# Performance work log

Measured on AMD Instinct MI355X. Metric: run time of the kernel, lower is better.

The kernel has to match this reference:

```python
import jax, jax.numpy as jnp
import numpy as np

B, S, H, D = 8, 1024, 16, 64  # batch, seq, heads, d_heads; hidden = H*D = 1024

def setup_inputs() -> dict:
    key = jax.random.key(0)
    ks = jax.random.split(key, 7)
    sc = 1.0 / np.sqrt(D)
    return {
        "sequences": jax.random.normal(ks[0], (B, S, H * D), dtype=jnp.float32),
        "Wq": jax.random.normal(ks[1], (H, D, D), dtype=jnp.float32) * sc,
        "bq": jax.random.normal(ks[2], (H, D), dtype=jnp.float32) * 0.01,
        "Wk": jax.random.normal(ks[3], (H, D, D), dtype=jnp.float32) * sc,
        "bk": jax.random.normal(ks[4], (H, D), dtype=jnp.float32) * 0.01,
        "Wv": jax.random.normal(ks[5], (H, D, D), dtype=jnp.float32) * sc,
        "bv": jax.random.normal(ks[6], (H, D), dtype=jnp.float32) * 0.01,
    }

def reference(sequences, Wq, bq, Wk, bk, Wv, bv):
    # sequences: [B, S, H*D] -> [B, S, H, D] (head h uses slice h*D:(h+1)*D)
    x = sequences.reshape(B, S, H, D)
    # per-head Linear: y = x @ W.T + b  (torch convention)
    q = jnp.einsum("bshd,hed->bshe", x, Wq) + bq
    k = jnp.einsum("bshd,hed->bshe", x, Wk) + bk
    v = jnp.einsum("bshd,hed->bshe", x, Wv) + bv
    scores = jnp.einsum("bqhd,bkhd->bhqk", q, k) / jnp.sqrt(jnp.float32(D))
    attn = jax.nn.softmax(scores, axis=-1)
    out = jnp.einsum("bhqk,bkhd->bqhd", attn, v)  # [B, S, H, D]
    return out.reshape(B, S, H * D)  # hstack over heads == reshape
```

## Files before the change

### kernel.cpp

```cpp
#include <hip/hip_runtime.h>
#include <hip/hip_bf16.h>


typedef __attribute__((ext_vector_type(8))) short short8;
typedef __attribute__((ext_vector_type(4))) float f32x4;
typedef __attribute__((ext_vector_type(16))) float f32x16;
typedef __attribute__((ext_vector_type(2))) unsigned int u32x2;
typedef __attribute__((ext_vector_type(4))) unsigned int u32x4;

#define MFMA32 __builtin_amdgcn_mfma_f32_32x32x16_bf16

#define QSCALE 0.1803368801111204f

__device__ __forceinline__ unsigned cvt_pk(float lo, float hi) {
  unsigned r;
  asm("v_cvt_pk_bf16_f32 %0, %1, %2" : "=v"(r) : "v"(lo), "v"(hi));
  return r;
}
__device__ __forceinline__ void pl32_swap(unsigned &a, unsigned &b) {
  asm("v_permlane32_swap_b32 %0, %1" : "+v"(a), "+v"(b));
}
__device__ __forceinline__ void pack_cd(const f32x16& p, short8& lo, short8& hi8) {
  unsigned d0 = cvt_pk(p[0],  p[1]);
  unsigned d2 = cvt_pk(p[4],  p[5]);
  pl32_swap(d0, d2);
  unsigned d1 = cvt_pk(p[2],  p[3]);
  unsigned d3 = cvt_pk(p[6],  p[7]);
  pl32_swap(d1, d3);
  u32x4 a = {d0, d1, d2, d3};
  unsigned e0 = cvt_pk(p[8],  p[9]);
  unsigned e2 = cvt_pk(p[12], p[13]);
  pl32_swap(e0, e2);
  unsigned e1 = cvt_pk(p[10], p[11]);
  unsigned e3 = cvt_pk(p[14], p[15]);
  pl32_swap(e1, e3);
  u32x4 b = {e0, e1, e2, e3};
  lo  = __builtin_bit_cast(short8, a);
  hi8 = __builtin_bit_cast(short8, b);
}
__device__ __forceinline__ void lds_barrier() {
  asm volatile("s_waitcnt lgkmcnt(0)" ::: "memory");
  __builtin_amdgcn_s_barrier();
}

__global__ __launch_bounds__(512) void kv_proj_kernel(
    const float* __restrict__ x,
    const float* __restrict__ Wk, const float* __restrict__ bk,
    const float* __restrict__ Wv, const float* __restrict__ bv,
    unsigned short* __restrict__ kv_ws)
{
  __shared__ unsigned short x_lds[128][72];
  __shared__ unsigned short wk_lds[64][72];
  __shared__ unsigned short wv_lds[64][72];

  const int h   = blockIdx.x & 15;
  const int tb  = blockIdx.x >> 4;
  const int tid = threadIdx.x;
  const int w   = tid >> 6;
  const int l   = tid & 63;
  const int hi  = l >> 5;
  const int cc  = l & 31;

  {
    const int r = tid >> 2, s = tid & 3;
    const float* xs = x + (size_t)(tb * 128 + r) * 1024 + h * 64 + s * 16;
    f32x4 v0 = *(const f32x4*)xs;
    f32x4 v1 = *(const f32x4*)(xs + 4);
    f32x4 v2 = *(const f32x4*)(xs + 8);
    f32x4 v3 = *(const f32x4*)(xs + 12);
    u32x4 d0 = {cvt_pk(v0[0], v0[1]), cvt_pk(v0[2], v0[3]),
                cvt_pk(v1[0], v1[1]), cvt_pk(v1[2], v1[3])};
    u32x4 d1 = {cvt_pk(v2[0], v2[1]), cvt_pk(v2[2], v2[3]),
                cvt_pk(v3[0], v3[1]), cvt_pk(v3[2], v3[3])};
    *(u32x4*)&x_lds[r][s * 16]     = d0;
    *(u32x4*)&x_lds[r][s * 16 + 8] = d1;
  }
  {
    const int r = tid >> 3, s = tid & 7;
    const float* wsk = Wk + (size_t)h * 4096 + r * 64 + s * 8;
    const float* wsv = Wv + (size_t)h * 4096 + r * 64 + s * 8;
    f32x4 k0 = *(const f32x4*)wsk;
    f32x4 k1 = *(const f32x4*)(wsk + 4);
    u32x4 dk = {cvt_pk(k0[0], k0[1]), cvt_pk(k0[2], k0[3]),
                cvt_pk(k1[0], k1[1]), cvt_pk(k1[2], k1[3])};
    *(u32x4*)&wk_lds[r][s * 8] = dk;
    f32x4 m0 = *(const f32x4*)wsv;
    f32x4 m1 = *(const f32x4*)(wsv + 4);
    u32x4 dv = {cvt_pk(m0[0], m0[1]), cvt_pk(m0[2], m0[3]),
                cvt_pk(m1[0], m1[1]), cvt_pk(m1[2], m1[3])};
    *(u32x4*)&wv_lds[r][s * 8] = dv;
  }
  __syncthreads();

  const int b = tb >> 3;
  unsigned short* kvt = kv_ws + (size_t)(b * 16 + h) * 131072
                              + (size_t)(tb & 7) * 16384;

  if (w < 4) {
    const int eb = w >> 1, cb = w & 1;
    const float* bkb = bk + h * 64 + eb * 32 + 4 * hi;
    f32x4 bk0 = *(const f32x4*)(bkb);
    f32x4 bk1 = *(const f32x4*)(bkb + 8);
    f32x4 bk2 = *(const f32x4*)(bkb + 16);
    f32x4 bk3 = *(const f32x4*)(bkb + 24);
#pragma unroll
    for (int sub = 0; sub < 2; ++sub) {
      f32x16 kkT = {};
#pragma unroll
      for (int ks = 0; ks < 4; ++ks) {
        short8 aW = *(const short8*)&wk_lds[eb * 32 + cc][ks * 16 + hi * 8];
        short8 bX = *(const short8*)&x_lds[sub * 64 + cb * 32 + cc][ks * 16 + hi * 8];
        kkT = MFMA32(aW, bX, kkT, 0, 0, 0);
      }
#pragma unroll
      for (int r = 0; r < 16; ++r) {
        const float bb = (r >> 2) == 0 ? bk0[r & 3] :
                         (r >> 2) == 1 ? bk1[r & 3] :
                         (r >> 2) == 2 ? bk2[r & 3] : bk3[r & 3];
        kkT[r] += bb;
      }
      short8 klo, khi;
      pack_cd(kkT, klo, khi);
      const int slot = 256 * eb + 64 * cb + l;
      *(short8*)&kvt[sub * 8192 + slot * 8]         = klo;
      *(short8*)&kvt[sub * 8192 + (slot + 128) * 8] = khi;
    }
  } else {
    const int tb32 = (w - 4) >> 1, db = (w - 4) & 1;
    const float bvv = bv[h * 64 + db * 32 + cc];
#pragma unroll
    for (int sub = 0; sub < 2; ++sub) {
      f32x16 vvC = {};
#pragma unroll
      for (int ks = 0; ks < 4; ++ks) {
        short8 aX = *(const short8*)&x_lds[sub * 64 + tb32 * 32 + cc][ks * 16 + hi * 8];
        short8 bW = *(const short8*)&wv_lds[db * 32 + cc][ks * 16 + hi * 8];
        vvC = MFMA32(aX, bW, vvC, 0, 0, 0);
      }
#pragma unroll
      for (int r = 0; r < 16; ++r) vvC[r] += bvv;
      short8 vlo, vhi;
      pack_cd(vvC, vlo, vhi);
      const int slot = 256 * tb32 + 64 * db + l;
      *(short8*)&kvt[sub * 8192 + 4096 + slot * 8]         = vlo;
      *(short8*)&kvt[sub * 8192 + 4096 + (slot + 128) * 8] = vhi;
    }
  }
}

__global__ __launch_bounds__(512, 4) void attn_kernel(
    const float* __restrict__ x,
    const float* __restrict__ Wq, const float* __restrict__ bq,
    const unsigned short* __restrict__ kv_ws,
    float* __restrict__ out)
{
  __shared__ __align__(16) char lds[32768];

  const int logical = (blockIdx.x & 7) * 64 + (blockIdx.x >> 3);
  const int qt = logical & 3;
  const int bh = logical >> 2;
  const int b  = bh >> 4;
  const int h  = bh & 15;
  const unsigned short* kvb = kv_ws + (size_t)bh * 131072;

  const int tid = threadIdx.x;
  const int w   = tid >> 6;
  const int l   = tid & 63;
  const int hi  = l >> 5;
  const int cc  = l & 31;

  const unsigned short* sgp = kvb + tid * 8;
  char* wbp = lds + tid * 16;

  short8 st[2];
#pragma unroll
  for (int j = 0; j < 2; ++j) st[j] = *(const short8*)(sgp + j * 4096);

  unsigned short* wq_l = (unsigned short*)lds;
  unsigned short* xh_l = (unsigned short*)(lds + 9216);

  {
    const int r = tid >> 3, s = tid & 7;
    const float* ws = Wq + h * 4096 + r * 64 + s * 8;
    f32x4 v0 = *(const f32x4*)ws;
    f32x4 v1 = *(const f32x4*)(ws + 4);
    u32x4 d = {cvt_pk(v0[0], v0[1]), cvt_pk(v0[2], v0[3]),
               cvt_pk(v1[0], v1[1]), cvt_pk(v1[2], v1[3])};
    *(u32x4*)&wq_l[r * 72 + s * 8] = d;
  }

  short8 qf[4];
  f32x16 qa0 = {}, qa1 = {};
#pragma unroll
  for (int p = 0; p < 2; ++p) {
    {
      const int r = tid >> 2, s = tid & 3;
      const float* xs = x + ((size_t)(b * 1024 + qt * 256 + p * 128 + r)) * 1024
                          + h * 64 + s * 16;
      f32x4 v0 = *(const f32x4*)xs;
      f32x4 v1 = *(const f32x4*)(xs + 4);
      f32x4 v2 = *(const f32x4*)(xs + 8);
      f32x4 v3 = *(const f32x4*)(xs + 12);
      u32x4 d0 = {cvt_pk(v0[0], v0[1]), cvt_pk(v0[2], v0[3]),
                  cvt_pk(v1[0], v1[1]), cvt_pk(v1[2], v1[3])};
      u32x4 d1 = {cvt_pk(v2[0], v2[1]), cvt_pk(v2[2], v2[3]),
                  cvt_pk(v3[0], v3[1]), cvt_pk(v3[2], v3[3])};
      *(u32x4*)&xh_l[r * 72 + s * 16]     = d0;
      *(u32x4*)&xh_l[r * 72 + s * 16 + 8] = d1;
    }
    lds_barrier();
    if ((w >> 2) == p) {
      const int tl = (w & 3) * 32 + cc;
#pragma unroll
      for (int c = 0; c < 4; ++c) {
        short8 xf  = *(const short8*)&xh_l[tl * 72 + c * 16 + hi * 8];
        short8 alo = *(const short8*)&wq_l[cc * 72 + c * 16 + hi * 8];
        short8 ahi = *(const short8*)&wq_l[(32 + cc) * 72 + c * 16 + hi * 8];
        qa0 = MFMA32(alo, xf, qa0, 0, 0, 0);
        qa1 = MFMA32(ahi, xf, qa1, 0, 0, 0);
      }
    }
    lds_barrier();
  }
  {
#pragma unroll
    for (int r = 0; r < 16; ++r) {
      const int e = (r & 3) + 8 * (r >> 2) + 4 * hi;
      qa0[r] = (qa0[r] + bq[h * 64 + e]) * QSCALE;
      qa1[r] = (qa1[r] + bq[h * 64 + 32 + e]) * QSCALE;
    }
    pack_cd(qa0, qf[0], qf[1]);
    pack_cd(qa1, qf[2], qf[3]);
  }

#pragma unroll
  for (int j = 0; j < 2; ++j) *(short8*)(wbp + j * 8192) = st[j];
#pragma unroll
  for (int j = 0; j < 2; ++j) st[j] = *(const short8*)(sgp + 8192 + j * 4096);
  lds_barrier();

  f32x16 ot0 = {}; f32x16 ot1 = {};
  float lsum = 0.f;

  for (int kv = 0; kv < 16; ++kv) {
    if (kv < 15) {
      char* d = wbp + ((kv + 1) & 1) * 16384;
#pragma unroll
      for (int j = 0; j < 2; ++j) *(short8*)(d + j * 8192) = st[j];
      if (kv < 14) {
        const unsigned short* s = sgp + (size_t)(kv + 2) * 8192;
#pragma unroll
        for (int j = 0; j < 2; ++j) st[j] = *(const short8*)(s + j * 4096);
      }
    }
    const char* kb_ = lds + (kv & 1) * 16384;
    const char* vb_ = kb_ + 8192;

    f32x16 s0 = {}; f32x16 s1 = {};
    __builtin_amdgcn_s_setprio(1);
#pragma unroll
    for (int c = 0; c < 4; ++c) {
      s0 = MFMA32(*(const short8*)(kb_ + (c * 128 + l) * 16),      qf[c], s0, 0, 0, 0);
      s1 = MFMA32(*(const short8*)(kb_ + (c * 128 + 64 + l) * 16), qf[c], s1, 0, 0, 0);
    }
    __builtin_amdgcn_s_setprio(0);

    float ps0 = 0.f, ps1 = 0.f;
#pragma unroll
    for (int i = 0; i < 16; ++i) { s0[i] = __builtin_amdgcn_exp2f(s0[i]); ps0 += s0[i]; }
#pragma unroll
    for (int i = 0; i < 16; ++i) { s1[i] = __builtin_amdgcn_exp2f(s1[i]); ps1 += s1[i]; }
    lsum += ps0 + ps1;

#pragma unroll
    for (int kb = 0; kb < 2; ++kb) {
      short8 pa0, pa1;
      pack_cd(kb ? s1 : s0, pa0, pa1);

      const int c20 = kb * 2, c21 = kb * 2 + 1;
      __builtin_amdgcn_s_setprio(1);
      ot0 = MFMA32(*(const short8*)(vb_ + (c20 * 128 + l) * 16),      pa0, ot0, 0, 0, 0);
      ot1 = MFMA32(*(const short8*)(vb_ + (c20 * 128 + 64 + l) * 16), pa0, ot1, 0, 0, 0);
      ot0 = MFMA32(*(const short8*)(vb_ + (c21 * 128 + l) * 16),      pa1, ot0, 0, 0, 0);
      ot1 = MFMA32(*(const short8*)(vb_ + (c21 * 128 + 64 + l) * 16), pa1, ot1, 0, 0, 0);
      __builtin_amdgcn_s_setprio(0);
    }
    lds_barrier();
  }

  const float lt  = lsum + __shfl_xor(lsum, 32, 64);
  const float inv = 1.0f / lt;
  const int s_row = qt * 256 + w * 32 + cc;
  float* op = out + ((size_t)(b * 1024 + s_row) << 10) + h * 64;
#pragma unroll
  for (int rg = 0; rg < 4; ++rg) {
    const int d0 = 8 * rg + 4 * hi;
    f32x4 v0, v1;
#pragma unroll
    for (int j = 0; j < 4; ++j) {
      v0[j] = ot0[rg * 4 + j] * inv;
      v1[j] = ot1[rg * 4 + j] * inv;
    }
    *(f32x4*)(op + d0)      = v0;
    *(f32x4*)(op + 32 + d0) = v1;
  }
}

extern "C" void kernel_launch(void* const* d_in, const int* in_sizes, int n_in,
                              void* d_out, int out_size, void* d_ws, size_t ws_size,
                              hipStream_t stream) {
  const float* x  = (const float*)d_in[0];
  const float* Wq = (const float*)d_in[1];
  const float* bq = (const float*)d_in[2];
  const float* Wk = (const float*)d_in[3];
  const float* bk = (const float*)d_in[4];
  const float* Wv = (const float*)d_in[5];
  const float* bv = (const float*)d_in[6];
  float* out = (float*)d_out;

  unsigned short* kv_ws = (unsigned short*)d_ws;

  kv_proj_kernel<<<1024, 512, 0, stream>>>(x, Wk, bk, Wv, bv, kv_ws);
  attn_kernel<<<512, 512, 0, stream>>>(x, Wq, bq, kv_ws, out);
}
```

Before: 67.21 us.

## Move Q projection into the projection kernel and load precomputed Q fragments

The Q projection moves out of the attention kernel into the first kernel, which now computes Q, K and V per 128-row tile, stores Q pre-scaled in bf16 fragment layout, and rebalances the work so all 8 waves do one tile of each. The attention kernel then loads Q fragments straight from workspace instead of reading x and Wq, converting them, and running an LDS-staged MFMA prologue with barriers. This shortens the attention kernel's prologue. In exchange it adds a bf16 Q round-trip through global memory (16 MB workspace) and more work and LDS in the projection kernel.

```diff
diff --git a/kernel.cpp b/kernel.cpp
--- a/kernel.cpp
+++ b/kernel.cpp
@@ -5,7 +5,6 @@
 typedef __attribute__((ext_vector_type(8))) short short8;
 typedef __attribute__((ext_vector_type(4))) float f32x4;
 typedef __attribute__((ext_vector_type(16))) float f32x16;
-typedef __attribute__((ext_vector_type(2))) unsigned int u32x2;
 typedef __attribute__((ext_vector_type(4))) unsigned int u32x4;
 
 #define MFMA32 __builtin_amdgcn_mfma_f32_32x32x16_bf16
@@ -43,13 +42,16 @@
   __builtin_amdgcn_s_barrier();
 }
 
-__global__ __launch_bounds__(512) void kv_proj_kernel(
+__global__ __launch_bounds__(512) void qkv_proj_kernel(
     const float* __restrict__ x,
+    const float* __restrict__ Wq, const float* __restrict__ bq,
     const float* __restrict__ Wk, const float* __restrict__ bk,
     const float* __restrict__ Wv, const float* __restrict__ bv,
+    unsigned short* __restrict__ q_ws,
     unsigned short* __restrict__ kv_ws)
 {
   __shared__ unsigned short x_lds[128][72];
+  __shared__ unsigned short wq_lds[64][72];
   __shared__ unsigned short wk_lds[64][72];
   __shared__ unsigned short wv_lds[64][72];
 
@@ -77,8 +79,14 @@
   }
   {
     const int r = tid >> 3, s = tid & 7;
+    const float* wsq = Wq + (size_t)h * 4096 + r * 64 + s * 8;
     const float* wsk = Wk + (size_t)h * 4096 + r * 64 + s * 8;
     const float* wsv = Wv + (size_t)h * 4096 + r * 64 + s * 8;
+    f32x4 q0 = *(const f32x4*)wsq;
+    f32x4 q1 = *(const f32x4*)(wsq + 4);
+    u32x4 dq = {cvt_pk(q0[0], q0[1]), cvt_pk(q0[2], q0[3]),
+                cvt_pk(q1[0], q1[1]), cvt_pk(q1[2], q1[3])};
+    *(u32x4*)&wq_lds[r][s * 8] = dq;
     f32x4 k0 = *(const f32x4*)wsk;
     f32x4 k1 = *(const f32x4*)(wsk + 4);
     u32x4 dk = {cvt_pk(k0[0], k0[1]), cvt_pk(k0[2], k0[3]),
@@ -93,64 +101,86 @@
   __syncthreads();
 
   const int b = tb >> 3;
-  unsigned short* kvt = kv_ws + (size_t)(b * 16 + h) * 131072
-                              + (size_t)(tb & 7) * 16384;
-
-  if (w < 4) {
-    const int eb = w >> 1, cb = w & 1;
-    const float* bkb = bk + h * 64 + eb * 32 + 4 * hi;
-    f32x4 bk0 = *(const f32x4*)(bkb);
-    f32x4 bk1 = *(const f32x4*)(bkb + 8);
-    f32x4 bk2 = *(const f32x4*)(bkb + 16);
-    f32x4 bk3 = *(const f32x4*)(bkb + 24);
-#pragma unroll
-    for (int sub = 0; sub < 2; ++sub) {
-      f32x16 kkT = {};
-#pragma unroll
-      for (int ks = 0; ks < 4; ++ks) {
-        short8 aW = *(const short8*)&wk_lds[eb * 32 + cc][ks * 16 + hi * 8];
-        short8 bX = *(const short8*)&x_lds[sub * 64 + cb * 32 + cc][ks * 16 + hi * 8];
-        kkT = MFMA32(aW, bX, kkT, 0, 0, 0);
-      }
-#pragma unroll
-      for (int r = 0; r < 16; ++r) {
-        const float bb = (r >> 2) == 0 ? bk0[r & 3] :
-                         (r >> 2) == 1 ? bk1[r & 3] :
-                         (r >> 2) == 2 ? bk2[r & 3] : bk3[r & 3];
-        kkT[r] += bb;
-      }
-      short8 klo, khi;
-      pack_cd(kkT, klo, khi);
-      const int slot = 256 * eb + 64 * cb + l;
-      *(short8*)&kvt[sub * 8192 + slot * 8]         = klo;
-      *(short8*)&kvt[sub * 8192 + (slot + 128) * 8] = khi;
-    }
-  } else {
-    const int tb32 = (w - 4) >> 1, db = (w - 4) & 1;
-    const float bvv = bv[h * 64 + db * 32 + cc];
-#pragma unroll
-    for (int sub = 0; sub < 2; ++sub) {
-      f32x16 vvC = {};
-#pragma unroll
-      for (int ks = 0; ks < 4; ++ks) {
-        short8 aX = *(const short8*)&x_lds[sub * 64 + tb32 * 32 + cc][ks * 16 + hi * 8];
-        short8 bW = *(const short8*)&wv_lds[db * 32 + cc][ks * 16 + hi * 8];
-        vvC = MFMA32(aX, bW, vvC, 0, 0, 0);
-      }
-#pragma unroll
-      for (int r = 0; r < 16; ++r) vvC[r] += bvv;
-      short8 vlo, vhi;
-      pack_cd(vvC, vlo, vhi);
-      const int slot = 256 * tb32 + 64 * db + l;
-      *(short8*)&kvt[sub * 8192 + 4096 + slot * 8]         = vlo;
-      *(short8*)&kvt[sub * 8192 + 4096 + (slot + 128) * 8] = vhi;
-    }
+  const int eb  = (w >> 2) & 1;
+  const int cb  = (w >> 1) & 1;
+  const int sub = w & 1;
+  const int tidx = (tb & 7) * 2 + sub;
+  unsigned short* kvt = kv_ws + (size_t)(b * 16 + h) * 131072 + (size_t)tidx * 8192;
+  unsigned short* qtt = q_ws  + (size_t)(b * 16 + h) * 65536  + (size_t)tidx * 4096;
+  const int slot = 256 * eb + 64 * cb + l;
+
+  {
+    f32x16 acc = {};
+#pragma unroll
+    for (int ks = 0; ks < 4; ++ks) {
+      short8 aW = *(const short8*)&wq_lds[eb * 32 + cc][ks * 16 + hi * 8];
+      short8 bX = *(const short8*)&x_lds[sub * 64 + cb * 32 + cc][ks * 16 + hi * 8];
+      acc = MFMA32(aW, bX, acc, 0, 0, 0);
+    }
+    const float* bb = bq + h * 64 + eb * 32 + 4 * hi;
+    f32x4 b0 = *(const f32x4*)(bb);
+    f32x4 b1 = *(const f32x4*)(bb + 8);
+    f32x4 b2 = *(const f32x4*)(bb + 16);
+    f32x4 b3 = *(const f32x4*)(bb + 24);
+#pragma unroll
+    for (int r = 0; r < 16; ++r) {
+      const float bz = (r >> 2) == 0 ? b0[r & 3] :
+                       (r >> 2) == 1 ? b1[r & 3] :
+                       (r >> 2) == 2 ? b2[r & 3] : b3[r & 3];
+      acc[r] = (acc[r] + bz) * QSCALE;
+    }
+    short8 lo, hi8;
+    pack_cd(acc, lo, hi8);
+    *(short8*)&qtt[slot * 8]         = lo;
+    *(short8*)&qtt[(slot + 128) * 8] = hi8;
+  }
+
+  {
+    f32x16 acc = {};
+#pragma unroll
+    for (int ks = 0; ks < 4; ++ks) {
+      short8 aW = *(const short8*)&wk_lds[eb * 32 + cc][ks * 16 + hi * 8];
+      short8 bX = *(const short8*)&x_lds[sub * 64 + cb * 32 + cc][ks * 16 + hi * 8];
+      acc = MFMA32(aW, bX, acc, 0, 0, 0);
+    }
+    const float* bb = bk + h * 64 + eb * 32 + 4 * hi;
+    f32x4 b0 = *(const f32x4*)(bb);
+    f32x4 b1 = *(const f32x4*)(bb + 8);
+    f32x4 b2 = *(const f32x4*)(bb + 16);
+    f32x4 b3 = *(const f32x4*)(bb + 24);
+#pragma unroll
+    for (int r = 0; r < 16; ++r) {
+      const float bz = (r >> 2) == 0 ? b0[r & 3] :
+                       (r >> 2) == 1 ? b1[r & 3] :
+                       (r >> 2) == 2 ? b2[r & 3] : b3[r & 3];
+      acc[r] += bz;
+    }
+    short8 lo, hi8;
+    pack_cd(acc, lo, hi8);
+    *(short8*)&kvt[slot * 8]         = lo;
+    *(short8*)&kvt[(slot + 128) * 8] = hi8;
+  }
+
+  {
+    f32x16 acc = {};
+#pragma unroll
+    for (int ks = 0; ks < 4; ++ks) {
+      short8 aX = *(const short8*)&x_lds[sub * 64 + eb * 32 + cc][ks * 16 + hi * 8];
+      short8 bW = *(const short8*)&wv_lds[cb * 32 + cc][ks * 16 + hi * 8];
+      acc = MFMA32(aX, bW, acc, 0, 0, 0);
+    }
+    const float bvv = bv[h * 64 + cb * 32 + cc];
+#pragma unroll
+    for (int r = 0; r < 16; ++r) acc[r] += bvv;
+    short8 lo, hi8;
+    pack_cd(acc, lo, hi8);
+    *(short8*)&kvt[4096 + slot * 8]         = lo;
+    *(short8*)&kvt[4096 + (slot + 128) * 8] = hi8;
   }
 }
 
 __global__ __launch_bounds__(512, 4) void attn_kernel(
-    const float* __restrict__ x,
-    const float* __restrict__ Wq, const float* __restrict__ bq,
+    const unsigned short* __restrict__ q_ws,
     const unsigned short* __restrict__ kv_ws,
     float* __restrict__ out)
 {
@@ -176,61 +206,14 @@
 #pragma unroll
   for (int j = 0; j < 2; ++j) st[j] = *(const short8*)(sgp + j * 4096);
 
-  unsigned short* wq_l = (unsigned short*)lds;
-  unsigned short* xh_l = (unsigned short*)(lds + 9216);
-
-  {
-    const int r = tid >> 3, s = tid & 7;
-    const float* ws = Wq + h * 4096 + r * 64 + s * 8;
-    f32x4 v0 = *(const f32x4*)ws;
-    f32x4 v1 = *(const f32x4*)(ws + 4);
-    u32x4 d = {cvt_pk(v0[0], v0[1]), cvt_pk(v0[2], v0[3]),
-               cvt_pk(v1[0], v1[1]), cvt_pk(v1[2], v1[3])};
-    *(u32x4*)&wq_l[r * 72 + s * 8] = d;
-  }
-
   short8 qf[4];
-  f32x16 qa0 = {}, qa1 = {};
-#pragma unroll
-  for (int p = 0; p < 2; ++p) {
-    {
-      const int r = tid >> 2, s = tid & 3;
-      const float* xs = x + ((size_t)(b * 1024 + qt * 256 + p * 128 + r)) * 1024
-                          + h * 64 + s * 16;
-      f32x4 v0 = *(const f32x4*)xs;
-      f32x4 v1 = *(const f32x4*)(xs + 4);
-      f32x4 v2 = *(const f32x4*)(xs + 8);
-      f32x4 v3 = *(const f32x4*)(xs + 12);
-      u32x4 d0 = {cvt_pk(v0[0], v0[1]), cvt_pk(v0[2], v0[3]),
-                  cvt_pk(v1[0], v1[1]), cvt_pk(v1[2], v1[3])};
-      u32x4 d1 = {cvt_pk(v2[0], v2[1]), cvt_pk(v2[2], v2[3]),
-                  cvt_pk(v3[0], v3[1]), cvt_pk(v3[2], v3[3])};
-      *(u32x4*)&xh_l[r * 72 + s * 16]     = d0;
-      *(u32x4*)&xh_l[r * 72 + s * 16 + 8] = d1;
-    }
-    lds_barrier();
-    if ((w >> 2) == p) {
-      const int tl = (w & 3) * 32 + cc;
-#pragma unroll
-      for (int c = 0; c < 4; ++c) {
-        short8 xf  = *(const short8*)&xh_l[tl * 72 + c * 16 + hi * 8];
-        short8 alo = *(const short8*)&wq_l[cc * 72 + c * 16 + hi * 8];
-        short8 ahi = *(const short8*)&wq_l[(32 + cc) * 72 + c * 16 + hi * 8];
-        qa0 = MFMA32(alo, xf, qa0, 0, 0, 0);
-        qa1 = MFMA32(ahi, xf, qa1, 0, 0, 0);
-      }
-    }
-    lds_barrier();
-  }
-  {
-#pragma unroll
-    for (int r = 0; r < 16; ++r) {
-      const int e = (r & 3) + 8 * (r >> 2) + 4 * hi;
-      qa0[r] = (qa0[r] + bq[h * 64 + e]) * QSCALE;
-      qa1[r] = (qa1[r] + bq[h * 64 + 32 + e]) * QSCALE;
-    }
-    pack_cd(qa0, qf[0], qf[1]);
-    pack_cd(qa1, qf[2], qf[3]);
+  {
+    const unsigned short* qp = q_ws + (size_t)bh * 65536
+                             + (size_t)(qt * 4 + (w >> 1)) * 4096
+                             + ((w & 1) * 64 + l) * 8;
+#pragma unroll
+    for (int c = 0; c < 4; ++c)
+      qf[c] = *(const short8*)(qp + c * 1024);
   }
 
 #pragma unroll
@@ -318,8 +301,10 @@
   const float* bv = (const float*)d_in[6];
   float* out = (float*)d_out;
 
-  unsigned short* kv_ws = (unsigned short*)d_ws;
-
-  kv_proj_kernel<<<1024, 512, 0, stream>>>(x, Wk, bk, Wv, bv, kv_ws);
-  attn_kernel<<<512, 512, 0, stream>>>(x, Wq, bq, kv_ws, out);
-}
+  unsigned short* q_ws  = (unsigned short*)d_ws;
+  unsigned short* kv_ws = q_ws + (size_t)8388608;
+
+  qkv_proj_kernel<<<1024, 512, 0, stream>>>(x, Wq, bq, Wk, bk, Wv, bv,
+                                            q_ws, kv_ws);
+  attn_kernel<<<512, 512, 0, stream>>>(q_ws, kv_ws, out);
+}
```

New measurement: 65.46 us, median of 3. 1.03x faster.
